# Kernel tuning notes

Measured on AMD Instinct MI355X. Metric: run time of the kernel, lower is better.

## Reference

```python
import jax, jax.numpy as jnp
import numpy as np

DIM = 64
NUM_GRAPHS = 256  # B: number of graphs in the batch (static)


def setup_inputs() -> dict:
    key = jax.random.key(0)
    ks = jax.random.split(key, 16)
    N, E = 8000, 40000

    def p(k, shape, s=0.1):
        return jax.random.normal(k, shape, jnp.float32) * s

    return dict(
        x=jax.random.normal(ks[0], (N, 21), jnp.float32),
        edge_attr=jax.random.uniform(ks[1], (E, 16), jnp.float32),
        edge_index=jax.random.randint(ks[2], (2, E), 0, N, jnp.int32),
        batch=jnp.sort(jax.random.randint(ks[3], (N,), 0, NUM_GRAPHS, jnp.int32)),
        lin0_w=p(ks[4], (DIM, 21)), lin0_b=jnp.zeros((DIM,), jnp.float32),
        nn_w1=p(ks[5], (128, 16)), nn_b1=jnp.zeros((128,), jnp.float32),
        nn_w2=p(ks[6], (DIM * DIM, 128), 0.02), nn_b2=jnp.zeros((DIM * DIM,), jnp.float32),
        conv_root=p(ks[7], (DIM, DIM)), conv_bias=jnp.zeros((DIM,), jnp.float32),
        gru_w_ih=p(ks[8], (3 * DIM, DIM)), gru_w_hh=p(ks[9], (3 * DIM, DIM)),
        gru_b_ih=jnp.zeros((3 * DIM,), jnp.float32), gru_b_hh=jnp.zeros((3 * DIM,), jnp.float32),
        lstm_w_ih=p(ks[10], (4 * DIM, 2 * DIM)), lstm_w_hh=p(ks[11], (4 * DIM, DIM)),
        lstm_b_ih=jnp.zeros((4 * DIM,), jnp.float32), lstm_b_hh=jnp.zeros((4 * DIM,), jnp.float32),
        lin1_w=p(ks[12], (DIM, 2 * DIM)), lin1_b=jnp.zeros((DIM,), jnp.float32),
        lin2_w=p(ks[13], (1, DIM)), lin2_b=jnp.zeros((1,), jnp.float32),
    )


def reference(x, edge_attr, edge_index, batch,
              lin0_w, lin0_b, nn_w1, nn_b1, nn_w2, nn_b2,
              conv_root, conv_bias, gru_w_ih, gru_w_hh, gru_b_ih, gru_b_hh,
              lstm_w_ih, lstm_w_hh, lstm_b_ih, lstm_b_hh,
              lin1_w, lin1_b, lin2_w, lin2_b):
    N = x.shape[0]
    src, dst = edge_index[0], edge_index[1]

    out = jax.nn.relu(x @ lin0_w.T + lin0_b)           # [N, 64]
    h = out

    # edge-conditioned weights (same every iteration): [E, 64, 64]
    e_h = jax.nn.relu(edge_attr @ nn_w1.T + nn_b1)
    w_e = (e_h @ nn_w2.T + nn_b2).reshape(-1, DIM, DIM)

    deg = jax.ops.segment_sum(jnp.ones_like(src, jnp.float32), dst, num_segments=N)
    deg = jnp.maximum(deg, 1.0)[:, None]

    for _ in range(3):
        # NNConv: gather + per-edge matmul + scatter-mean + root/bias
        msg = jnp.einsum('ei,eio->eo', out[src], w_e)  # [E, 64]
        agg = jax.ops.segment_sum(msg, dst, num_segments=N) / deg
        m = jax.nn.relu(agg + out @ conv_root + conv_bias)
        # GRU cell (seq_len = 1), torch gate order r, z, n
        gi = m @ gru_w_ih.T + gru_b_ih
        gh = h @ gru_w_hh.T + gru_b_hh
        ir, iz, i_n = jnp.split(gi, 3, axis=-1)
        hr, hz, h_n = jnp.split(gh, 3, axis=-1)
        r = jax.nn.sigmoid(ir + hr)
        z = jax.nn.sigmoid(iz + hz)
        n = jnp.tanh(i_n + r * h_n)
        h = (1.0 - z) * n + z * h
        out = h

    # Set2Set pooling, 3 processing steps
    B = NUM_GRAPHS
    q_star = jnp.zeros((B, 2 * DIM), x.dtype)
    hs = jnp.zeros((B, DIM), x.dtype)
    cs = jnp.zeros((B, DIM), x.dtype)
    for _ in range(3):
        gates = q_star @ lstm_w_ih.T + lstm_b_ih + hs @ lstm_w_hh.T + lstm_b_hh
        gi_, gf_, gg_, go_ = jnp.split(gates, 4, axis=-1)  # torch gate order i,f,g,o
        cs = jax.nn.sigmoid(gf_) * cs + jax.nn.sigmoid(gi_) * jnp.tanh(gg_)
        hs = jax.nn.sigmoid(go_) * jnp.tanh(cs)
        q = hs                                             # [B, 64]
        e = jnp.sum(out * q[batch], axis=-1)               # [N]
        mmax = jax.ops.segment_max(e, batch, num_segments=B)
        ex = jnp.exp(e - mmax[batch])
        s = jax.ops.segment_sum(ex, batch, num_segments=B)
        a = ex / s[batch]
        r_read = jax.ops.segment_sum(a[:, None] * out, batch, num_segments=B)
        q_star = jnp.concatenate([q, r_read], axis=-1)     # [B, 128]

    y = jax.nn.relu(q_star @ lin1_w.T + lin1_b)
    y = y @ lin2_w.T + lin2_b
    return y.reshape(-1)
```

## Files before the change

kernel.cpp:

```cpp
#include <hip/hip_runtime.h>
#include <math.h>

#define NN 8000
#define NE 40000
#define NGB 256
#define SK 8192
#define KSPLIT 16

typedef unsigned int u32;
typedef unsigned short u16;
typedef __attribute__((ext_vector_type(8))) short short8v;
typedef __attribute__((ext_vector_type(4))) float float4v;
typedef __attribute__((ext_vector_type(4))) unsigned int uint4v;

__device__ __forceinline__ float sigmoidf_(float x) { return 1.f / (1.f + expf(-x)); }

__device__ __forceinline__ u32 bf16_rne(float f) {
    u32 x = __builtin_bit_cast(u32, f);
    return (x + 0x7FFFu + ((x >> 16) & 1u)) >> 16;
}

__device__ __forceinline__ uint4v pack_bf8(const float v[8]) {
    u32 h[8];
#pragma unroll
    for (int j = 0; j < 8; ++j) h[j] = bf16_rne(v[j]);
    return (uint4v){ h[0] | (h[1] << 16), h[2] | (h[3] << 16),
                     h[4] | (h[5] << 16), h[6] | (h[7] << 16) };
}

__device__ __forceinline__ void pack8(const float* p, float scale, short8v& ah, short8v& al) {
    float v[8];
#pragma unroll
    for (int j = 0; j < 8; ++j) v[j] = p[j];
    u32 hu[8], lu[8];
#pragma unroll
    for (int j = 0; j < 8; ++j) {
        float s = v[j] * scale;
        hu[j] = bf16_rne(s);
        float fh = __builtin_bit_cast(float, hu[j] << 16);
        lu[j] = bf16_rne(s - fh);
    }
    uint4v hset = { hu[0] | (hu[1] << 16), hu[2] | (hu[3] << 16),
                    hu[4] | (hu[5] << 16), hu[6] | (hu[7] << 16) };
    uint4v lset = { lu[0] | (lu[1] << 16), lu[2] | (lu[3] << 16),
                    lu[4] | (lu[5] << 16), lu[6] | (lu[7] << 16) };
    ah = __builtin_bit_cast(short8v, hset);
    al = __builtin_bit_cast(short8v, lset);
}

__global__ __launch_bounds__(256) void k_eh(
    const float* __restrict__ ea, const float* __restrict__ w1,
    const float* __restrict__ b1, float* __restrict__ e_h) {
    __shared__ float w1s[2048];
    __shared__ float b1s[128];
    int t = threadIdx.x;
#pragma unroll
    for (int i = 0; i < 8; ++i) w1s[i * 256 + t] = w1[i * 256 + t];
    if (t < 128) b1s[t] = b1[t];
    __syncthreads();
    int e = blockIdx.x * 32 + (t & 31);
    int j0 = (t >> 5) * 16;
    const float4* ea4 = (const float4*)ea;
    float4 a0 = ea4[(size_t)e * 4 + 0], a1 = ea4[(size_t)e * 4 + 1];
    float4 a2 = ea4[(size_t)e * 4 + 2], a3 = ea4[(size_t)e * 4 + 3];
    float av[16] = {a0.x, a0.y, a0.z, a0.w, a1.x, a1.y, a1.z, a1.w,
                    a2.x, a2.y, a2.z, a2.w, a3.x, a3.y, a3.z, a3.w};
    float res[16];
#pragma unroll
    for (int jj = 0; jj < 16; ++jj) {
        int j = j0 + jj;
        float s = b1s[j];
#pragma unroll
        for (int c = 0; c < 16; ++c) s += av[c] * w1s[j * 16 + c];
        res[jj] = fmaxf(s, 0.f);
    }
    float4* op = (float4*)&e_h[(size_t)e * 128 + j0];
#pragma unroll
    for (int q = 0; q < 4; ++q)
        op[q] = make_float4(res[q * 4], res[q * 4 + 1], res[q * 4 + 2], res[q * 4 + 3]);
}

#define SETUP_LIN0 (NN * 64)
#define SETUP_W2   (64 * SK)
#define SETUP_MW   8192
#define SETUP_GB   24576
#define SETUP_G    (NGB + 1)
#define SETUP_TOTAL (SETUP_LIN0 + SETUP_W2 + SETUP_MW + SETUP_GB + SETUP_G + NN)
__global__ void k_setup(const float* __restrict__ x, const float* __restrict__ lin0_w,
                        const float* __restrict__ lin0_b,
                        const float* __restrict__ nn_w2, const float* __restrict__ conv_root,
                        const float* __restrict__ nn_b2, const float* __restrict__ gw_ih,
                        const float* __restrict__ gw_hh, const int* __restrict__ batch,
                        float* __restrict__ out,
                        u16* __restrict__ Whi, u16* __restrict__ Wlo,
                        u16* __restrict__ Bmh, u16* __restrict__ Bml,
                        u16* __restrict__ Bih_h, u16* __restrict__ Bih_l,
                        u16* __restrict__ Bhh_h, u16* __restrict__ Bhh_l,
                        int* __restrict__ gstart, int* __restrict__ degi) {
    int idx = blockIdx.x * 256 + threadIdx.x;
    if (idx < SETUP_LIN0) {
        int n = idx >> 6, o = idx & 63;
        float s = lin0_b[o];
#pragma unroll
        for (int c = 0; c < 21; ++c) s += x[n * 21 + c] * lin0_w[o * 21 + c];
        out[idx] = fmaxf(s, 0.f);
        return;
    }
    idx -= SETUP_LIN0;
    if (idx < SETUP_W2) {
        int o = idx >> 13, kap = idx & 8191;
        int i = kap >> 7, k = kap & 127;
        float v = nn_w2[(size_t)((i << 6) + o) * 128 + k];
        u32 h = bf16_rne(v);
        float fh = __builtin_bit_cast(float, h << 16);
        u32 l = bf16_rne(v - fh);
        int pos = ((kap >> 3) * 64 + o) * 8 + (kap & 7);
        Whi[pos] = (u16)h; Wlo[pos] = (u16)l;
        return;
    }
    idx -= SETUP_W2;
    if (idx < SETUP_MW) {
        int k = idx >> 6, o = idx & 63;
        float v = (k < 64) ? nn_b2[k * 64 + o] : conv_root[(k - 64) * 64 + o];
        u32 h = bf16_rne(v);
        float fh = __builtin_bit_cast(float, h << 16);
        u32 l = bf16_rne(v - fh);
        int pos = ((k >> 3) * 64 + o) * 8 + (k & 7);
        Bmh[pos] = (u16)h; Bml[pos] = (u16)l;
        return;
    }
    idx -= SETUP_MW;
    if (idx < SETUP_GB) {
        int half = idx >= 12288;
        int i2 = idx - half * 12288;
        int o = i2 % 192, k = i2 / 192;
        float v = half ? gw_hh[o * 64 + k] : gw_ih[o * 64 + k];
        u32 h = bf16_rne(v);
        float fh = __builtin_bit_cast(float, h << 16);
        u32 l = bf16_rne(v - fh);
        int pos = ((k >> 3) * 192 + o) * 8 + (k & 7);
        if (half) { Bhh_h[pos] = (u16)h; Bhh_l[pos] = (u16)l; }
        else      { Bih_h[pos] = (u16)h; Bih_l[pos] = (u16)l; }
        return;
    }
    idx -= SETUP_GB;
    if (idx < SETUP_G) {
        int g = idx;
        int lo = 0, hi = NN;
        while (lo < hi) { int mid = (lo + hi) >> 1; if (batch[mid] < g) lo = mid + 1; else hi = mid; }
        gstart[g] = lo;
        return;
    }
    idx -= SETUP_G;
    if (idx < NN) degi[idx] = 0;
}

__global__ void k_deg(const int* __restrict__ dst, int* __restrict__ degi) {
    int e = blockIdx.x * blockDim.x + threadIdx.x;
    if (e < NE) atomicAdd(&degi[dst[e]], 1);
}

__global__ __launch_bounds__(1024) void k_scan(
    const int* __restrict__ degi, int* __restrict__ rowptr,
    int* __restrict__ cursor, float* __restrict__ degf) {
    __shared__ int tsum[1024];
    int t = threadIdx.x;
    int base = t * 8;
    int v[8];
    int s = 0;
#pragma unroll
    for (int j = 0; j < 8; ++j) {
        int i = base + j;
        v[j] = (i < NN) ? degi[i] : 0;
        s += v[j];
    }
    tsum[t] = s;
    __syncthreads();
    for (int off = 1; off < 1024; off <<= 1) {
        int add = (t >= off) ? tsum[t - off] : 0;
        __syncthreads();
        tsum[t] += add;
        __syncthreads();
    }
    int exc = (t == 0) ? 0 : tsum[t - 1];
#pragma unroll
    for (int j = 0; j < 8; ++j) {
        int i = base + j;
        if (i < NN) {
            rowptr[i] = exc; cursor[i] = exc;
            degf[i] = (float)(v[j] > 1 ? v[j] : 1);
            exc += v[j];
        }
    }
    if (t == 1023) rowptr[NN] = tsum[1023];
}

__global__ void k_fill(const int* __restrict__ dst, int* __restrict__ cursor,
                       int* __restrict__ elist) {
    int e = blockIdx.x * blockDim.x + threadIdx.x;
    if (e < NE) { int p = atomicAdd(&cursor[dst[e]], 1); elist[p] = e; }
}

__global__ __launch_bounds__(256) void k_sbuild(
    const float* __restrict__ out, const float* __restrict__ e_h,
    const int* __restrict__ src, const int* __restrict__ rowptr,
    const int* __restrict__ elist, u16* __restrict__ S_bf,
    float* __restrict__ Osum, int base) {
    int t = threadIdx.x;
    int n = base + blockIdx.x;
    int ig = t >> 4;
    int k8 = t & 15;
    int lane = t & 63;
    float acc[4][8];
#pragma unroll
    for (int j = 0; j < 4; ++j)
#pragma unroll
        for (int c = 0; c < 8; ++c) acc[j][c] = 0.f;
    float osum = 0.f;
    int r0 = rowptr[n], r1 = rowptr[n + 1];
    const float4* out4 = (const float4*)out;
    const float4* eh4p = (const float4*)e_h;
    for (int idx = r0; idx < r1; ++idx) {
        int e = elist[idx];
        int sn = src[e];
        float4 e0 = eh4p[(size_t)e * 32 + k8 * 2];
        float4 e1 = eh4p[(size_t)e * 32 + k8 * 2 + 1];
        float ehv[8] = {e0.x, e0.y, e0.z, e0.w, e1.x, e1.y, e1.z, e1.w};
        float4 f = out4[sn * 16 + ig];
        float fv[4] = {f.x, f.y, f.z, f.w};
#pragma unroll
        for (int j = 0; j < 4; ++j)
#pragma unroll
            for (int c = 0; c < 8; ++c) acc[j][c] += fv[j] * ehv[c];
        if (t < 64) osum += out[(size_t)sn * 64 + lane];
    }
    uint4v* S4 = (uint4v*)S_bf;
    size_t rb = (size_t)blockIdx.x * (SK / 8);
#pragma unroll
    for (int j = 0; j < 4; ++j)
        S4[rb + (size_t)(ig * 4 + j) * 16 + k8] = pack_bf8(acc[j]);
    if (t < 64) Osum[(size_t)n * 64 + lane] = osum;
}

__global__ __launch_bounds__(64) void k_gemm(
    const u16* __restrict__ S_bf, const u16* __restrict__ Whi,
    const u16* __restrict__ Wlo, float* __restrict__ P, int base) {
    int lane = threadIdx.x;
    int lrow = lane & 15, lkg = lane >> 4;
    int m0 = blockIdx.x * 32;
    int ks = blockIdx.y;
    int kbase = ks * (SK / KSPLIT);
    float4v acc[2][4];
#pragma unroll
    for (int ms = 0; ms < 2; ++ms)
#pragma unroll
        for (int nt = 0; nt < 4; ++nt) acc[ms][nt] = (float4v){0.f, 0.f, 0.f, 0.f};
    const short8v* bhv = (const short8v*)Whi;
    const short8v* blv = (const short8v*)Wlo;
    const u16* ar0 = S_bf + (size_t)(m0 + lrow) * SK + kbase + lkg * 8;
    const u16* ar1 = ar0 + (size_t)16 * SK;
    int kc0 = (kbase >> 3) + lkg;

#pragma unroll 4
    for (int kk = 0; kk < SK / KSPLIT / 32; ++kk) {
        short8v ah0 = *(const short8v*)(ar0 + kk * 32);
        short8v ah1 = *(const short8v*)(ar1 + kk * 32);
        int bo = (kc0 + kk * 4) * 64 + lrow;
        short8v bh[4], bl[4];
#pragma unroll
        for (int nt = 0; nt < 4; ++nt) { bh[nt] = bhv[bo + nt * 16]; bl[nt] = blv[bo + nt * 16]; }
#pragma unroll
        for (int nt = 0; nt < 4; ++nt) {
            acc[0][nt] = __builtin_amdgcn_mfma_f32_16x16x32_bf16(ah0, bh[nt], acc[0][nt], 0, 0, 0);
            acc[0][nt] = __builtin_amdgcn_mfma_f32_16x16x32_bf16(ah0, bl[nt], acc[0][nt], 0, 0, 0);
            acc[1][nt] = __builtin_amdgcn_mfma_f32_16x16x32_bf16(ah1, bh[nt], acc[1][nt], 0, 0, 0);
            acc[1][nt] = __builtin_amdgcn_mfma_f32_16x16x32_bf16(ah1, bl[nt], acc[1][nt], 0, 0, 0);
        }
    }
    int gbase = base + m0;
#pragma unroll
    for (int ms = 0; ms < 2; ++ms)
#pragma unroll
        for (int nt = 0; nt < 4; ++nt)
#pragma unroll
            for (int jj = 0; jj < 4; ++jj) {
                int row = ms * 16 + lkg * 4 + jj;
                int o = nt * 16 + lrow;
                P[((size_t)ks * NN + gbase + row) * 64 + o] = acc[ms][nt][jj];
            }
}

__global__ __launch_bounds__(64) void k_node(
    float* __restrict__ out, const float* __restrict__ P,
    const float* __restrict__ Osum, const float* __restrict__ degf,
    const u16* __restrict__ Bmh, const u16* __restrict__ Bml,
    const u16* __restrict__ Bih_h, const u16* __restrict__ Bih_l,
    const u16* __restrict__ Bhh_h, const u16* __restrict__ Bhh_l,
    const float* __restrict__ conv_bias,
    const float* __restrict__ gb_ih, const float* __restrict__ gb_hh) {
    __shared__ float lds[16][68];
    int lane = threadIdx.x;
    int lrow = lane & 15, lkg = lane >> 4;
    int n0 = blockIdx.x * 16;
    int arow = n0 + lrow;

    {
        const float4* P4 = (const float4*)P;
        float4 ps[4];
#pragma unroll
        for (int c = 0; c < 4; ++c) ps[c] = make_float4(0.f, 0.f, 0.f, 0.f);
        for (int p = 0; p < KSPLIT; ++p) {
#pragma unroll
            for (int c = 0; c < 4; ++c) {
                float4 v = P4[(size_t)p * (NN * 16) + (size_t)arow * 16 + lkg * 4 + c];
                ps[c].x += v.x; ps[c].y += v.y; ps[c].z += v.z; ps[c].w += v.w;
            }
        }
#pragma unroll
        for (int c = 0; c < 4; ++c)
            *(float4*)&lds[lrow][lkg * 16 + c * 4] = ps[c];
    }
    __syncthreads();

    float invd = 1.f / degf[arow];
    float4v acc[4];
#pragma unroll
    for (int nt = 0; nt < 4; ++nt) acc[nt] = (float4v){0.f, 0.f, 0.f, 0.f};
    const short8v* bhv = (const short8v*)Bmh;
    const short8v* blv = (const short8v*)Bml;
#pragma unroll
    for (int s = 0; s < 4; ++s) {
        short8v ah, al;
        if (s < 2) pack8(&Osum[(size_t)arow * 64 + s * 32 + lkg * 8], invd, ah, al);
        else       pack8(&out[(size_t)arow * 64 + (s - 2) * 32 + lkg * 8], 1.f, ah, al);
        int kc = s * 4 + lkg;
#pragma unroll
        for (int nt = 0; nt < 4; ++nt) {
            short8v bh = bhv[kc * 64 + nt * 16 + lrow];
            short8v bl = blv[kc * 64 + nt * 16 + lrow];
            acc[nt] = __builtin_amdgcn_mfma_f32_16x16x32_bf16(ah, bh, acc[nt], 0, 0, 0);
            acc[nt] = __builtin_amdgcn_mfma_f32_16x16x32_bf16(al, bh, acc[nt], 0, 0, 0);
            acc[nt] = __builtin_amdgcn_mfma_f32_16x16x32_bf16(ah, bl, acc[nt], 0, 0, 0);
        }
    }
    float invd2[4];
#pragma unroll
    for (int jj = 0; jj < 4; ++jj) invd2[jj] = 1.f / degf[n0 + lkg * 4 + jj];
    float mval[4][4];
#pragma unroll
    for (int nt = 0; nt < 4; ++nt) {
        int o = nt * 16 + lrow;
        float cb = conv_bias[o];
#pragma unroll
        for (int jj = 0; jj < 4; ++jj)
            mval[nt][jj] = fmaxf(acc[nt][jj] + lds[lkg * 4 + jj][o] * invd2[jj] + cb, 0.f);
    }
    __syncthreads();
#pragma unroll
    for (int nt = 0; nt < 4; ++nt)
#pragma unroll
        for (int jj = 0; jj < 4; ++jj)
            lds[lkg * 4 + jj][nt * 16 + lrow] = mval[nt][jj];
    __syncthreads();

    float4v ai[12], ah_[12];
#pragma unroll
    for (int nt = 0; nt < 12; ++nt) { ai[nt] = (float4v){0.f, 0.f, 0.f, 0.f}; ah_[nt] = (float4v){0.f, 0.f, 0.f, 0.f}; }
    const short8v* bih_h = (const short8v*)Bih_h;
    const short8v* bih_l = (const short8v*)Bih_l;
    const short8v* bhh_h = (const short8v*)Bhh_h;
    const short8v* bhh_l = (const short8v*)Bhh_l;
#pragma unroll
    for (int s = 0; s < 2; ++s) {
        short8v mh, ml, hh, hl;
        pack8(&lds[lrow][s * 32 + lkg * 8], 1.f, mh, ml);
        pack8(&out[(size_t)arow * 64 + s * 32 + lkg * 8], 1.f, hh, hl);
        int kc = s * 4 + lkg;
#pragma unroll
        for (int nt = 0; nt < 12; ++nt) {
            int bo = kc * 192 + nt * 16 + lrow;
            short8v b1 = bih_h[bo], b2 = bih_l[bo];
            ai[nt] = __builtin_amdgcn_mfma_f32_16x16x32_bf16(mh, b1, ai[nt], 0, 0, 0);
            ai[nt] = __builtin_amdgcn_mfma_f32_16x16x32_bf16(ml, b1, ai[nt], 0, 0, 0);
            ai[nt] = __builtin_amdgcn_mfma_f32_16x16x32_bf16(mh, b2, ai[nt], 0, 0, 0);
            short8v b3 = bhh_h[bo], b4 = bhh_l[bo];
            ah_[nt] = __builtin_amdgcn_mfma_f32_16x16x32_bf16(hh, b3, ah_[nt], 0, 0, 0);
            ah_[nt] = __builtin_amdgcn_mfma_f32_16x16x32_bf16(hl, b3, ah_[nt], 0, 0, 0);
            ah_[nt] = __builtin_amdgcn_mfma_f32_16x16x32_bf16(hh, b4, ah_[nt], 0, 0, 0);
        }
    }
#pragma unroll
    for (int nt = 0; nt < 4; ++nt) {
        int o = nt * 16 + lrow;
        float bi0 = gb_ih[o], bi1 = gb_ih[64 + o], bi2 = gb_ih[128 + o];
        float bh0 = gb_hh[o], bh1 = gb_hh[64 + o], bh2 = gb_hh[128 + o];
#pragma unroll
        for (int jj = 0; jj < 4; ++jj) {
            int row = n0 + lkg * 4 + jj;
            float ir = ai[nt][jj] + bi0,  hr = ah_[nt][jj] + bh0;
            float iz = ai[nt + 4][jj] + bi1, hz = ah_[nt + 4][jj] + bh1;
            float in_ = ai[nt + 8][jj] + bi2, hn = ah_[nt + 8][jj] + bh2;
            float r = sigmoidf_(ir + hr);
            float z = sigmoidf_(iz + hz);
            float nv = tanhf(in_ + r * hn);
            float ho = out[(size_t)row * 64 + o];
            out[(size_t)row * 64 + o] = (1.f - z) * nv + z * ho;
        }
    }
}

__global__ __launch_bounds__(256) void k_s2s(
    const float* __restrict__ out, const int* __restrict__ gstart,
    const float* __restrict__ lw_ih, const float* __restrict__ lw_hh,
    const float* __restrict__ lb_ih, const float* __restrict__ lb_hh,
    const float* __restrict__ lin1_w, const float* __restrict__ lin1_b,
    const float* __restrict__ lin2_w, const float* __restrict__ lin2_b,
    float* __restrict__ yout) {
    __shared__ float qs[128], hsL[64], csL[64], gates[256];
    __shared__ float pv[384];
    __shared__ float red[4][64];
    __shared__ float sswv[4], mmaxw[4];
    int g = blockIdx.x, t = threadIdx.x, wv = t >> 6, lane = t & 63;
    int s0 = gstart[g], s1 = gstart[g + 1];
    if (t < 128) qs[t] = 0.f;
    if (t < 64) { hsL[t] = 0.f; csL[t] = 0.f; }
    __syncthreads();
    for (int st = 0; st < 3; ++st) {
        float s = lb_ih[t] + lb_hh[t];
        const float4* wi = (const float4*)&lw_ih[t * 128];
#pragma unroll
        for (int i = 0; i < 32; ++i) {
            float4 a = wi[i];
            s += qs[i * 4] * a.x + qs[i * 4 + 1] * a.y + qs[i * 4 + 2] * a.z + qs[i * 4 + 3] * a.w;
        }
        const float4* wh = (const float4*)&lw_hh[t * 64];
#pragma unroll
        for (int i = 0; i < 16; ++i) {
            float4 a = wh[i];
            s += hsL[i * 4] * a.x + hsL[i * 4 + 1] * a.y + hsL[i * 4 + 2] * a.z + hsL[i * 4 + 3] * a.w;
        }
        gates[t] = s;
        __syncthreads();
        if (t < 64) {
            float ig = sigmoidf_(gates[t]);
            float fg = sigmoidf_(gates[64 + t]);
            float gg = tanhf(gates[128 + t]);
            float og = sigmoidf_(gates[192 + t]);
            float c = fg * csL[t] + ig * gg;
            csL[t] = c;
            hsL[t] = og * tanhf(c);
        }
        __syncthreads();
        float wmax = -1e30f;
        for (int i = s0 + wv; i < s1; i += 4) {
            float p = out[(size_t)i * 64 + lane] * hsL[lane];
#pragma unroll
            for (int off = 32; off >= 1; off >>= 1) p += __shfl_xor(p, off);
            if (lane == 0) pv[i - s0] = p;
            wmax = fmaxf(wmax, p);
        }
        if (lane == 0) mmaxw[wv] = wmax;
        __syncthreads();
        float mmax = fmaxf(fmaxf(mmaxw[0], mmaxw[1]), fmaxf(mmaxw[2], mmaxw[3]));
        float ssum = 0.f, racc = 0.f;
        for (int i = s0 + wv; i < s1; i += 4) {
            float w = expf(pv[i - s0] - mmax);
            ssum += w;
            racc += w * out[(size_t)i * 64 + lane];
        }
        red[wv][lane] = racc;
        if (lane == 0) sswv[wv] = ssum;
        __syncthreads();
        if (t < 64) {
            float rt = red[0][t] + red[1][t] + red[2][t] + red[3][t];
            float stot = sswv[0] + sswv[1] + sswv[2] + sswv[3];
            qs[t] = hsL[t];
            qs[64 + t] = (s1 > s0) ? rt / stot : 0.f;
        }
        __syncthreads();
    }
    if (t < 64) {
        float s = lin1_b[t];
        const float4* w1 = (const float4*)&lin1_w[t * 128];
#pragma unroll
        for (int i = 0; i < 32; ++i) {
            float4 a = w1[i];
            s += qs[i * 4] * a.x + qs[i * 4 + 1] * a.y + qs[i * 4 + 2] * a.z + qs[i * 4 + 3] * a.w;
        }
        s = fmaxf(s, 0.f) * lin2_w[t];
#pragma unroll
        for (int off = 32; off >= 1; off >>= 1) s += __shfl_xor(s, off);
        if (t == 0) yout[g] = s + lin2_b[0];
    }
}

extern "C" void kernel_launch(void* const* d_in, const int* in_sizes, int n_in,
                              void* d_out, int out_size, void* d_ws, size_t ws_size,
                              hipStream_t stream) {
    (void)in_sizes; (void)n_in; (void)out_size;
    const float* x        = (const float*)d_in[0];
    const float* eattr    = (const float*)d_in[1];
    const int*   ei       = (const int*)d_in[2];
    const int*   batch    = (const int*)d_in[3];
    const float* lin0_w   = (const float*)d_in[4];
    const float* lin0_b   = (const float*)d_in[5];
    const float* nn_w1    = (const float*)d_in[6];
    const float* nn_b1    = (const float*)d_in[7];
    const float* nn_w2    = (const float*)d_in[8];
    const float* nn_b2    = (const float*)d_in[9];
    const float* conv_root= (const float*)d_in[10];
    const float* conv_bias= (const float*)d_in[11];
    const float* gw_ih    = (const float*)d_in[12];
    const float* gw_hh    = (const float*)d_in[13];
    const float* gb_ih    = (const float*)d_in[14];
    const float* gb_hh    = (const float*)d_in[15];
    const float* lw_ih    = (const float*)d_in[16];
    const float* lw_hh    = (const float*)d_in[17];
    const float* lb_ih    = (const float*)d_in[18];
    const float* lb_hh    = (const float*)d_in[19];
    const float* lin1_w   = (const float*)d_in[20];
    const float* lin1_b   = (const float*)d_in[21];
    const float* lin2_w   = (const float*)d_in[22];
    const float* lin2_b   = (const float*)d_in[23];
    const int* src = ei;
    const int* dst = ei + NE;

    char* w = (char*)d_ws;
    auto alloc = [&](size_t bytes) { char* p = w; w += (bytes + 255) & ~(size_t)255; return p; };
    float* out    = (float*)alloc((size_t)NN * 64 * 4);
    float* e_h    = (float*)alloc((size_t)NE * 128 * 4);
    u16*   Whi    = (u16*)alloc((size_t)64 * SK * 2);
    u16*   Wlo    = (u16*)alloc((size_t)64 * SK * 2);
    float* P      = (float*)alloc((size_t)KSPLIT * NN * 64 * 4);
    float* Osum   = (float*)alloc((size_t)NN * 64 * 4);
    u16*   Bmh    = (u16*)alloc((size_t)8192 * 2);
    u16*   Bml    = (u16*)alloc((size_t)8192 * 2);
    u16*   Bih_h  = (u16*)alloc((size_t)12288 * 2);
    u16*   Bih_l  = (u16*)alloc((size_t)12288 * 2);
    u16*   Bhh_h  = (u16*)alloc((size_t)12288 * 2);
    u16*   Bhh_l  = (u16*)alloc((size_t)12288 * 2);
    float* degf   = (float*)alloc((size_t)NN * 4);
    int*   degi   = (int*)alloc((size_t)NN * 4);
    int*   rowptr = (int*)alloc((size_t)(NN + 1) * 4);
    int*   cursor = (int*)alloc((size_t)(NN + 1) * 4);
    int*   elist  = (int*)alloc((size_t)NE * 4);
    int*   gstart = (int*)alloc((size_t)(NGB + 1) * 4);
    size_t used = (size_t)(w - (char*)d_ws);
    size_t avail = ws_size > used ? ws_size - used : 0;
    size_t maxrows = avail / ((size_t)SK * 2);
    int chunkN = maxrows > (size_t)NN ? NN : (int)maxrows;
    chunkN = (chunkN / 64) * 64;
    if (chunkN < 64) chunkN = 64;
    u16* S_bf = (u16*)w;

    k_setup<<<(SETUP_TOTAL + 255) / 256, 256, 0, stream>>>(
        x, lin0_w, lin0_b, nn_w2, conv_root, nn_b2,
        gw_ih, gw_hh, batch, out, Whi, Wlo, Bmh, Bml,
        Bih_h, Bih_l, Bhh_h, Bhh_l, gstart, degi);
    k_eh<<<NE / 32, 256, 0, stream>>>(eattr, nn_w1, nn_b1, e_h);
    k_deg<<<(NE + 255) / 256, 256, 0, stream>>>(dst, degi);
    k_scan<<<1, 1024, 0, stream>>>(degi, rowptr, cursor, degf);
    k_fill<<<(NE + 255) / 256, 256, 0, stream>>>(dst, cursor, elist);

    for (int it = 0; it < 3; ++it) {
        for (int cb = 0; cb < NN; cb += chunkN) {
            int cn = (NN - cb) < chunkN ? (NN - cb) : chunkN;
            k_sbuild<<<cn, 256, 0, stream>>>(out, e_h, src, rowptr, elist, S_bf, Osum, cb);
            k_gemm<<<dim3(cn / 32, KSPLIT), 64, 0, stream>>>(S_bf, Whi, Wlo, P, cb);
        }
        k_node<<<NN / 16, 64, 0, stream>>>(out, P, Osum, degf, Bmh, Bml,
                                           Bih_h, Bih_l, Bhh_h, Bhh_l,
                                           conv_bias, gb_ih, gb_hh);
    }

    k_s2s<<<NGB, 256, 0, stream>>>(out, gstart, lw_ih, lw_hh, lb_ih, lb_hh,
                                   lin1_w, lin1_b, lin2_w, lin2_b, (float*)d_out);
}
```

Measured before the change: 363.7 us.

## Store split-K GEMM partials as bf16 and preload A fragments

The split-K GEMM now writes its partial sums to P as bf16 instead of fp32, halving the partial-sum write traffic and the matching read traffic in the node kernel, which now unpacks and sums bf16 pairs. The GEMM also preloads all 16 A-operand fragments into registers before the MFMA loop and requests two blocks per SIMD through launch bounds. Rounding 16 partials to bf16 before summing adds error on top of the existing hi/lo bf16 weight split, and the larger register footprint could spill or cap occupancy.

```diff
diff --git a/kernel.cpp b/kernel.cpp
--- a/kernel.cpp
+++ b/kernel.cpp
@@ -242,9 +242,9 @@
     if (t < 64) Osum[(size_t)n * 64 + lane] = osum;
 }
 
-__global__ __launch_bounds__(64) void k_gemm(
+__global__ __launch_bounds__(64, 2) void k_gemm(
     const u16* __restrict__ S_bf, const u16* __restrict__ Whi,
-    const u16* __restrict__ Wlo, float* __restrict__ P, int base) {
+    const u16* __restrict__ Wlo, u16* __restrict__ P, int base) {
     int lane = threadIdx.x;
     int lrow = lane & 15, lkg = lane >> 4;
     int m0 = blockIdx.x * 32;
@@ -261,20 +261,24 @@
     const u16* ar1 = ar0 + (size_t)16 * SK;
     int kc0 = (kbase >> 3) + lkg;
 
+    short8v a0s[16], a1s[16];
+#pragma unroll
+    for (int kk = 0; kk < 16; ++kk) {
+        a0s[kk] = *(const short8v*)(ar0 + kk * 32);
+        a1s[kk] = *(const short8v*)(ar1 + kk * 32);
+    }
 #pragma unroll 4
-    for (int kk = 0; kk < SK / KSPLIT / 32; ++kk) {
-        short8v ah0 = *(const short8v*)(ar0 + kk * 32);
-        short8v ah1 = *(const short8v*)(ar1 + kk * 32);
+    for (int kk = 0; kk < 16; ++kk) {
         int bo = (kc0 + kk * 4) * 64 + lrow;
         short8v bh[4], bl[4];
 #pragma unroll
         for (int nt = 0; nt < 4; ++nt) { bh[nt] = bhv[bo + nt * 16]; bl[nt] = blv[bo + nt * 16]; }
 #pragma unroll
         for (int nt = 0; nt < 4; ++nt) {
-            acc[0][nt] = __builtin_amdgcn_mfma_f32_16x16x32_bf16(ah0, bh[nt], acc[0][nt], 0, 0, 0);
-            acc[0][nt] = __builtin_amdgcn_mfma_f32_16x16x32_bf16(ah0, bl[nt], acc[0][nt], 0, 0, 0);
-            acc[1][nt] = __builtin_amdgcn_mfma_f32_16x16x32_bf16(ah1, bh[nt], acc[1][nt], 0, 0, 0);
-            acc[1][nt] = __builtin_amdgcn_mfma_f32_16x16x32_bf16(ah1, bl[nt], acc[1][nt], 0, 0, 0);
+            acc[0][nt] = __builtin_amdgcn_mfma_f32_16x16x32_bf16(a0s[kk], bh[nt], acc[0][nt], 0, 0, 0);
+            acc[0][nt] = __builtin_amdgcn_mfma_f32_16x16x32_bf16(a0s[kk], bl[nt], acc[0][nt], 0, 0, 0);
+            acc[1][nt] = __builtin_amdgcn_mfma_f32_16x16x32_bf16(a1s[kk], bh[nt], acc[1][nt], 0, 0, 0);
+            acc[1][nt] = __builtin_amdgcn_mfma_f32_16x16x32_bf16(a1s[kk], bl[nt], acc[1][nt], 0, 0, 0);
         }
     }
     int gbase = base + m0;
@@ -286,12 +290,12 @@
             for (int jj = 0; jj < 4; ++jj) {
                 int row = ms * 16 + lkg * 4 + jj;
                 int o = nt * 16 + lrow;
-                P[((size_t)ks * NN + gbase + row) * 64 + o] = acc[ms][nt][jj];
+                P[((size_t)ks * NN + gbase + row) * 64 + o] = (u16)bf16_rne(acc[ms][nt][jj]);
             }
 }
 
 __global__ __launch_bounds__(64) void k_node(
-    float* __restrict__ out, const float* __restrict__ P,
+    float* __restrict__ out, const u16* __restrict__ P,
     const float* __restrict__ Osum, const float* __restrict__ degf,
     const u16* __restrict__ Bmh, const u16* __restrict__ Bml,
     const u16* __restrict__ Bih_h, const u16* __restrict__ Bih_l,
@@ -305,20 +309,21 @@
     int arow = n0 + lrow;
 
     {
-        const float4* P4 = (const float4*)P;
-        float4 ps[4];
-#pragma unroll
-        for (int c = 0; c < 4; ++c) ps[c] = make_float4(0.f, 0.f, 0.f, 0.f);
+        float ps[16];
+#pragma unroll
+        for (int c = 0; c < 16; ++c) ps[c] = 0.f;
         for (int p = 0; p < KSPLIT; ++p) {
-#pragma unroll
-            for (int c = 0; c < 4; ++c) {
-                float4 v = P4[(size_t)p * (NN * 16) + (size_t)arow * 16 + lkg * 4 + c];
-                ps[c].x += v.x; ps[c].y += v.y; ps[c].z += v.z; ps[c].w += v.w;
+            const uint4v* Pp = (const uint4v*)(P + (size_t)p * (NN * 64) + (size_t)arow * 64 + lkg * 16);
+            uint4v v0 = Pp[0], v1 = Pp[1];
+            u32 wv[8] = {v0.x, v0.y, v0.z, v0.w, v1.x, v1.y, v1.z, v1.w};
+#pragma unroll
+            for (int q = 0; q < 8; ++q) {
+                ps[q * 2]     += __builtin_bit_cast(float, wv[q] << 16);
+                ps[q * 2 + 1] += __builtin_bit_cast(float, wv[q] & 0xFFFF0000u);
             }
         }
 #pragma unroll
-        for (int c = 0; c < 4; ++c)
-            *(float4*)&lds[lrow][lkg * 16 + c * 4] = ps[c];
+        for (int c = 0; c < 16; ++c) lds[lrow][lkg * 16 + c] = ps[c];
     }
     __syncthreads();
 
@@ -531,7 +536,7 @@
     float* e_h    = (float*)alloc((size_t)NE * 128 * 4);
     u16*   Whi    = (u16*)alloc((size_t)64 * SK * 2);
     u16*   Wlo    = (u16*)alloc((size_t)64 * SK * 2);
-    float* P      = (float*)alloc((size_t)KSPLIT * NN * 64 * 4);
+    u16*   P      = (u16*)alloc((size_t)KSPLIT * NN * 64 * 2);
     float* Osum   = (float*)alloc((size_t)NN * 64 * 4);
     u16*   Bmh    = (u16*)alloc((size_t)8192 * 2);
     u16*   Bml    = (u16*)alloc((size_t)8192 * 2);
```

New measurement: 626.1 us. 1.72x slower.
